# Optimization experiments

Measured on AMD Instinct MI355X. Metric: run time of the kernel, lower is better.

Reference implementation:

```python
import jax, jax.numpy as jnp
import numpy as np

B, NCH, NT = 64, 129, 200
D_MODEL, D_STATE, D_CONV, HEADDIM, NLAYERS = 256, 16, 4, 32, 4
D_INNER = 2 * D_MODEL            # expand=2 -> 512
NHEADS = D_INNER // HEADDIM      # 16
CONV_DIM = D_INNER + 2 * D_STATE # 544 (ngroups=1)
D_IN_PROJ = 2 * D_INNER + 2 * D_STATE + NHEADS  # 1072


def silu(x):
    return x * jax.nn.sigmoid(x)


def layernorm(x, w, b, eps=1e-5):
    m = x.mean(-1, keepdims=True)
    v = ((x - m) ** 2).mean(-1, keepdims=True)
    return (x - m) * jax.lax.rsqrt(v + eps) * w + b


def dwconv(x, w, b, pad):
    # x: (B, C, T), w: (C, K) depthwise, pad: (left, right)
    y = jax.lax.conv_general_dilated(x, w[:, None, :], (1,), [pad],
                                     feature_group_count=x.shape[1])
    return y + b[None, :, None]


def mamba2_block(u, Wi, cw, cb, dtb, Alog, Dh, nw, Wo):
    # u: (b, l, d_model)
    b, l, _ = u.shape
    zxbcdt = u @ Wi.T  # (b, l, 1072)
    z, xBC, dt = jnp.split(zxbcdt, [D_INNER, D_INNER + CONV_DIM], axis=-1)
    dt = jax.nn.softplus(dt + dtb)  # (b, l, nheads)
    # causal depthwise conv + silu on xBC
    xBC = silu(dwconv(xBC.transpose(0, 2, 1), cw, cb, (D_CONV - 1, 0)).transpose(0, 2, 1))
    xh, Bm, Cm = jnp.split(xBC, [D_INNER, D_INNER + D_STATE], axis=-1)
    xh = xh.reshape(b, l, NHEADS, HEADDIM)
    A = -jnp.exp(Alog)              # (h,)
    dA = jnp.exp(dt * A)            # (b, l, h)
    dtx = dt[..., None] * xh        # (b, l, h, p)

    def step(hst, inp):
        dA_t, dtx_t, B_t, C_t = inp
        hst = dA_t[:, :, None, None] * hst + dtx_t[..., None] * B_t[:, None, None, :]
        y_t = jnp.einsum('bhpn,bn->bhp', hst, C_t)
        return hst, y_t

    h0 = jnp.zeros((b, NHEADS, HEADDIM, D_STATE), u.dtype)
    _, ys = jax.lax.scan(step, h0, (dA.swapaxes(0, 1), dtx.swapaxes(0, 1),
                                    Bm.swapaxes(0, 1), Cm.swapaxes(0, 1)))
    y = ys.swapaxes(0, 1) + xh * Dh[None, None, :, None]  # (b, l, h, p)
    y = y.reshape(b, l, D_INNER)
    # gated RMSNorm (norm_before_gate=False): gate first, then rmsnorm
    y = y * silu(z)
    y = y * jax.lax.rsqrt((y * y).mean(-1, keepdims=True) + 1e-5) * nw
    return y @ Wo.T


def setup_inputs() -> dict:
    key = jax.random.key(0)
    ks = iter(jax.random.split(key, 32))
    nrm = lambda shape, s=0.02: jax.random.normal(next(ks), shape, jnp.float32) * s
    dt0 = jax.random.uniform(next(ks), (NLAYERS, NHEADS), minval=1e-3, maxval=0.1)
    return {
        'x': jax.random.normal(next(ks), (B, NCH, NT), jnp.float32),
        'emb': nrm((NCH, D_MODEL), 1.0),
        'sconv_w': nrm((NCH, 3), 0.3),
        'sconv_b': jnp.zeros((NCH,), jnp.float32),
        'mixer_w': nrm((D_MODEL, NCH), 0.05),
        'mixer_b': jnp.zeros((D_MODEL,), jnp.float32),
        'enc_ln_w': jnp.ones((D_MODEL,), jnp.float32),
        'enc_ln_b': jnp.zeros((D_MODEL,), jnp.float32),
        'in_proj_w': nrm((NLAYERS, D_IN_PROJ, D_MODEL)),
        'conv_w': nrm((NLAYERS, CONV_DIM, D_CONV), 0.3),
        'conv_b': jnp.zeros((NLAYERS, CONV_DIM), jnp.float32),
        'dt_bias': jnp.log(jnp.expm1(dt0)),
        'A_log': jnp.log(jax.random.uniform(next(ks), (NLAYERS, NHEADS), minval=1.0, maxval=16.0)),
        'D_skip': jnp.ones((NLAYERS, NHEADS), jnp.float32),
        'norm_w': jnp.ones((NLAYERS, D_INNER), jnp.float32),
        'out_proj_w': nrm((NLAYERS, D_MODEL, D_INNER)),
        'ln_w': jnp.ones((NLAYERS, D_MODEL), jnp.float32),
        'ln_b': jnp.zeros((NLAYERS, D_MODEL), jnp.float32),
        'head1_w': nrm((D_MODEL // 2, D_MODEL), 0.05),
        'head1_b': jnp.zeros((D_MODEL // 2,), jnp.float32),
        'head2_w': nrm((1, D_MODEL // 2), 0.05),
        'head2_b': jnp.zeros((1,), jnp.float32),
    }


def reference(x, emb, sconv_w, sconv_b, mixer_w, mixer_b, enc_ln_w, enc_ln_b,
              in_proj_w, conv_w, conv_b, dt_bias, A_log, D_skip, norm_w,
              out_proj_w, ln_w, ln_b, head1_w, head1_b, head2_w, head2_b):
    # SpatialChannelEncoder: depthwise conv over time + channel-mixing Linear
    xs = dwconv(x, sconv_w, sconv_b, (1, 1))                  # (b, c, t)
    h = jnp.einsum('bct,dc->btd', xs, mixer_w) + mixer_b      # (b, t, d)
    h = h + emb.mean(0)                                       # mean channel embedding
    h = layernorm(h, enc_ln_w, enc_ln_b)                      # dropout=identity (eval)
    # Stacked Mamba2 blocks with post-norm residual
    for i in range(NLAYERS):
        res = h
        y = mamba2_block(h, in_proj_w[i], conv_w[i], conv_b[i], dt_bias[i],
                         A_log[i], D_skip[i], norm_w[i], out_proj_w[i])
        h = layernorm(y + res, ln_w[i], ln_b[i])
    pooled = h.mean(1)                                        # AdaptiveAvgPool1d(1)
    hid = jax.nn.relu(pooled @ head1_w.T + head1_b)
    return hid @ head2_w.T + head2_b                          # (b, 1)
```

## Files before the change

kernel.cpp:

```cpp
#include <hip/hip_runtime.h>
#include <math.h>

#define B_   64
#define T_   200
#define DM   256
#define DI   512
#define NH   16
#define HD   32
#define DSZ  16
#define CD   544
#define DIP  1072
#define M_TOT (B_*T_)
#define NCH_ 129
#define KENC 192
#define NCHUNK 10
#define CLEN  20
#define NBC  48

typedef unsigned short u16;
typedef unsigned int u32;
typedef _Float16 f16;
typedef __attribute__((ext_vector_type(8))) _Float16 half8;
typedef __attribute__((ext_vector_type(4))) short short4v;
typedef __attribute__((ext_vector_type(4))) float f32x4;
typedef __attribute__((ext_vector_type(2))) float f32x2;

__device__ __forceinline__ float wave_sum(float v) {
    #pragma unroll
    for (int off = 32; off > 0; off >>= 1) v += __shfl_xor(v, off);
    return v;
}
__device__ __forceinline__ u16 f16bits(float a) {
    f16 h = (f16)a;
    return __builtin_bit_cast(u16, h);
}
__device__ __forceinline__ float f16tof(u16 v) {
    return (float)__builtin_bit_cast(f16, v);
}

__global__ void emb_mean_k(const float* __restrict__ emb, float* __restrict__ em) {
    int d = threadIdx.x;
    float s = 0.f;
    for (int c = 0; c < NCH_; ++c) s += emb[c * DM + d];
    em[d] = s * (1.f / NCH_);
}

__global__ void xsA2_k(const float* __restrict__ x, const float* __restrict__ w,
                       const float* __restrict__ b, u16* __restrict__ A2) {
    int idx = blockIdx.x * blockDim.x + threadIdx.x;
    if (idx >= M_TOT * KENC) return;
    int c = idx % KENC;
    int m = idx / KENC;
    float acc = 0.f;
    if (c < NCH_) {
        int t = m % T_;
        int bb = m / T_;
        const float* xr = x + (size_t)(bb * NCH_ + c) * T_;
        acc = b[c];
        if (t > 0)      acc += w[c*3+0] * xr[t-1];
        acc += w[c*3+1] * xr[t];
        if (t < T_-1)   acc += w[c*3+2] * xr[t+1];
    }
    A2[(size_t)m * KENC + c] = f16bits(acc);
}

__global__ void pack_b2s_k(const float* __restrict__ W, u16* __restrict__ B2,
                           int L, int N, int Npad, int Kreal, int K) {
    int idx = blockIdx.x * blockDim.x + threadIdx.x;
    if (idx >= L * Npad * K) return;
    int k = idx % K;
    int n = (idx / K) % Npad;
    int l = idx / (K * Npad);
    u16 hi = 0;
    if (n < N && k < Kreal)
        hi = f16bits(W[((size_t)l * N + n) * Kreal + k]);
    B2[((size_t)l * Npad + n) * K + k] = hi;
}

__global__ __launch_bounds__(256) void gemm_m64n128h(const u16* __restrict__ A2,
                                                     const u16* __restrict__ B2,
                                                     u16* __restrict__ C,
                                                     int K2, int ldc, int Nreal,
                                                     int nbx) {
    __shared__ u16 As[64 * 64];
    __shared__ u16 Bs[128 * 64];
    int nwg = gridDim.x;
    int lin = blockIdx.x;
    int q = nwg >> 3, r = nwg & 7;
    int xcd = lin & 7, idx = lin >> 3;
    int wg = ((xcd < r) ? xcd * (q + 1) : r * (q + 1) + (xcd - r) * q) + idx;
    int bx = wg % nbx, by = wg / nbx;

    int tid = threadIdx.x;
    int lane = tid & 63;
    int wave = tid >> 6;
    int wr = wave >> 1;
    int wc = wave & 1;
    int bm = by * 64;
    int bn = bx * 128;

    f32x4 acc[2][4] = {};
    const size_t ldA = (size_t)K2 * 2;

    for (int k0 = 0; k0 < K2; k0 += 64) {
        #pragma unroll
        for (int c = 0; c < 2; ++c) {
            int o = c * 4096 + tid * 16;
            int row = o >> 7;
            int slot = (o >> 4) & 7;
            int ss = slot ^ (row & 7);
            const char* src = (const char*)A2 + (size_t)(bm + row) * ldA
                              + (size_t)k0 * 2 + ss * 16;
            __builtin_amdgcn_global_load_lds(
                (const __attribute__((address_space(1))) u32*)src,
                (__attribute__((address_space(3))) u32*)((char*)As + o),
                16, 0, 0);
        }
        #pragma unroll
        for (int c = 0; c < 4; ++c) {
            int o = c * 4096 + tid * 16;
            int row = o >> 7;
            int slot = (o >> 4) & 7;
            int ss = slot ^ (row & 7);
            const char* src = (const char*)B2 + (size_t)(bn + row) * ldA
                              + (size_t)k0 * 2 + ss * 16;
            __builtin_amdgcn_global_load_lds(
                (const __attribute__((address_space(1))) u32*)src,
                (__attribute__((address_space(3))) u32*)((char*)Bs + o),
                16, 0, 0);
        }
        __syncthreads();
        #pragma unroll
        for (int kk = 0; kk < 2; ++kk) {
            int lslot = kk * 4 + (lane >> 4);
            half8 afr[2], bfr[4];
            #pragma unroll
            for (int n = 0; n < 4; ++n) {
                int row = wc * 64 + n * 16 + (lane & 15);
                int ps = lslot ^ (row & 7);
                bfr[n] = *(const half8*)((const char*)Bs + row * 128 + ps * 16);
            }
            #pragma unroll
            for (int m = 0; m < 2; ++m) {
                int row = wr * 32 + m * 16 + (lane & 15);
                int ps = lslot ^ (row & 7);
                afr[m] = *(const half8*)((const char*)As + row * 128 + ps * 16);
            }
            #pragma unroll
            for (int m = 0; m < 2; ++m)
                #pragma unroll
                for (int n = 0; n < 4; ++n)
                    acc[m][n] = __builtin_amdgcn_mfma_f32_16x16x32_f16(
                        bfr[n], afr[m], acc[m][n], 0, 0, 0);
        }
        __syncthreads();
    }

    int crow0 = bm + wr * 32;
    int ccol0 = bn + wc * 64;
    #pragma unroll
    for (int m = 0; m < 2; ++m) {
        int row = crow0 + m * 16 + (lane & 15);
        #pragma unroll
        for (int n = 0; n < 4; ++n) {
            int col = ccol0 + n * 16 + (lane >> 4) * 4;
            if (col < Nreal) {
                short4v hv;
                #pragma unroll
                for (int j = 0; j < 4; ++j) hv[j] = (short)f16bits(acc[m][n][j]);
                *(short4v*)(C + (size_t)row * ldc + col) = hv;
            }
        }
    }
}

__global__ __launch_bounds__(256) void gemm_m64n64(const u16* __restrict__ A2,
                                                   const u16* __restrict__ B2,
                                                   float* __restrict__ C,
                                                   int K2, int ldc, int Nreal,
                                                   int nbx) {
    __shared__ u16 As[64 * 64];
    __shared__ u16 Bs[64 * 64];
    int nwg = gridDim.x;
    int lin = blockIdx.x;
    int q = nwg >> 3, r = nwg & 7;
    int xcd = lin & 7, idx = lin >> 3;
    int wg = ((xcd < r) ? xcd * (q + 1) : r * (q + 1) + (xcd - r) * q) + idx;
    int bx = wg % nbx, by = wg / nbx;

    int tid = threadIdx.x;
    int lane = tid & 63;
    int wave = tid >> 6;
    int wr = wave >> 1;
    int wc = wave & 1;
    int bm = by * 64;
    int bn = bx * 64;

    f32x4 acc[2][2] = {};
    const size_t ldA = (size_t)K2 * 2;

    for (int k0 = 0; k0 < K2; k0 += 64) {
        #pragma unroll
        for (int c = 0; c < 2; ++c) {
            int o = c * 4096 + tid * 16;
            int row = o >> 7;
            int slot = (o >> 4) & 7;
            int ss = slot ^ (row & 7);
            const char* src = (const char*)A2 + (size_t)(bm + row) * ldA
                              + (size_t)k0 * 2 + ss * 16;
            __builtin_amdgcn_global_load_lds(
                (const __attribute__((address_space(1))) u32*)src,
                (__attribute__((address_space(3))) u32*)((char*)As + o),
                16, 0, 0);
        }
        #pragma unroll
        for (int c = 0; c < 2; ++c) {
            int o = c * 4096 + tid * 16;
            int row = o >> 7;
            int slot = (o >> 4) & 7;
            int ss = slot ^ (row & 7);
            const char* src = (const char*)B2 + (size_t)(bn + row) * ldA
                              + (size_t)k0 * 2 + ss * 16;
            __builtin_amdgcn_global_load_lds(
                (const __attribute__((address_space(1))) u32*)src,
                (__attribute__((address_space(3))) u32*)((char*)Bs + o),
                16, 0, 0);
        }
        __syncthreads();
        #pragma unroll
        for (int kk = 0; kk < 2; ++kk) {
            int lslot = kk * 4 + (lane >> 4);
            half8 afr[2], bfr[2];
            #pragma unroll
            for (int n = 0; n < 2; ++n) {
                int row = wc * 32 + n * 16 + (lane & 15);
                int ps = lslot ^ (row & 7);
                bfr[n] = *(const half8*)((const char*)Bs + row * 128 + ps * 16);
            }
            #pragma unroll
            for (int m = 0; m < 2; ++m) {
                int row = wr * 32 + m * 16 + (lane & 15);
                int ps = lslot ^ (row & 7);
                afr[m] = *(const half8*)((const char*)As + row * 128 + ps * 16);
            }
            #pragma unroll
            for (int m = 0; m < 2; ++m)
                #pragma unroll
                for (int n = 0; n < 2; ++n)
                    acc[m][n] = __builtin_amdgcn_mfma_f32_16x16x32_f16(
                        bfr[n], afr[m], acc[m][n], 0, 0, 0);
        }
        __syncthreads();
    }

    int crow0 = bm + wr * 32;
    int ccol0 = bn + wc * 32;
    #pragma unroll
    for (int m = 0; m < 2; ++m) {
        int row = crow0 + m * 16 + (lane & 15);
        #pragma unroll
        for (int n = 0; n < 2; ++n) {
            int col = ccol0 + n * 16 + (lane >> 4) * 4;
            if (col < Nreal)
                *(f32x4*)(C + (size_t)row * ldc + col) = acc[m][n];
        }
    }
}

__global__ __launch_bounds__(256) void gemm_m64n64h(const u16* __restrict__ A2,
                                                    const u16* __restrict__ B2,
                                                    u16* __restrict__ C,
                                                    int K2, int ldc, int Nreal,
                                                    int nbx) {
    __shared__ u16 As[64 * 64];
    __shared__ u16 Bs[64 * 64];
    int nwg = gridDim.x;
    int lin = blockIdx.x;
    int q = nwg >> 3, r = nwg & 7;
    int xcd = lin & 7, idx = lin >> 3;
    int wg = ((xcd < r) ? xcd * (q + 1) : r * (q + 1) + (xcd - r) * q) + idx;
    int bx = wg % nbx, by = wg / nbx;

    int tid = threadIdx.x;
    int lane = tid & 63;
    int wave = tid >> 6;
    int wr = wave >> 1;
    int wc = wave & 1;
    int bm = by * 64;
    int bn = bx * 64;

    f32x4 acc[2][2] = {};
    const size_t ldA = (size_t)K2 * 2;

    for (int k0 = 0; k0 < K2; k0 += 64) {
        #pragma unroll
        for (int c = 0; c < 2; ++c) {
            int o = c * 4096 + tid * 16;
            int row = o >> 7;
            int slot = (o >> 4) & 7;
            int ss = slot ^ (row & 7);
            const char* src = (const char*)A2 + (size_t)(bm + row) * ldA
                              + (size_t)k0 * 2 + ss * 16;
            __builtin_amdgcn_global_load_lds(
                (const __attribute__((address_space(1))) u32*)src,
                (__attribute__((address_space(3))) u32*)((char*)As + o),
                16, 0, 0);
        }
        #pragma unroll
        for (int c = 0; c < 2; ++c) {
            int o = c * 4096 + tid * 16;
            int row = o >> 7;
            int slot = (o >> 4) & 7;
            int ss = slot ^ (row & 7);
            const char* src = (const char*)B2 + (size_t)(bn + row) * ldA
                              + (size_t)k0 * 2 + ss * 16;
            __builtin_amdgcn_global_load_lds(
                (const __attribute__((address_space(1))) u32*)src,
                (__attribute__((address_space(3))) u32*)((char*)Bs + o),
                16, 0, 0);
        }
        __syncthreads();
        #pragma unroll
        for (int kk = 0; kk < 2; ++kk) {
            int lslot = kk * 4 + (lane >> 4);
            half8 afr[2], bfr[2];
            #pragma unroll
            for (int n = 0; n < 2; ++n) {
                int row = wc * 32 + n * 16 + (lane & 15);
                int ps = lslot ^ (row & 7);
                bfr[n] = *(const half8*)((const char*)Bs + row * 128 + ps * 16);
            }
            #pragma unroll
            for (int m = 0; m < 2; ++m) {
                int row = wr * 32 + m * 16 + (lane & 15);
                int ps = lslot ^ (row & 7);
                afr[m] = *(const half8*)((const char*)As + row * 128 + ps * 16);
            }
            #pragma unroll
            for (int m = 0; m < 2; ++m)
                #pragma unroll
                for (int n = 0; n < 2; ++n)
                    acc[m][n] = __builtin_amdgcn_mfma_f32_16x16x32_f16(
                        bfr[n], afr[m], acc[m][n], 0, 0, 0);
        }
        __syncthreads();
    }

    int crow0 = bm + wr * 32;
    int ccol0 = bn + wc * 32;
    #pragma unroll
    for (int m = 0; m < 2; ++m) {
        int row = crow0 + m * 16 + (lane & 15);
        #pragma unroll
        for (int n = 0; n < 2; ++n) {
            int col = ccol0 + n * 16 + (lane >> 4) * 4;
            if (col < Nreal) {
                short4v hv;
                #pragma unroll
                for (int j = 0; j < 4; ++j) hv[j] = (short)f16bits(acc[m][n][j]);
                *(short4v*)(C + (size_t)row * ldc + col) = hv;
            }
        }
    }
}

__global__ __launch_bounds__(256) void enc_ln_k(float* __restrict__ h,
        const float* __restrict__ mb, const float* __restrict__ em,
        const float* __restrict__ w, const float* __restrict__ bb,
        u16* __restrict__ A2) {
    int row = blockIdx.x * 4 + (threadIdx.x >> 6);
    int lane = threadIdx.x & 63;
    int e = lane * 4;
    float* hr = h + (size_t)row * DM;
    f32x4 v = *(const f32x4*)(hr + e);
    f32x4 vm = *(const f32x4*)(mb + e);
    f32x4 ve = *(const f32x4*)(em + e);
    float s = 0.f, sq = 0.f;
    #pragma unroll
    for (int j = 0; j < 4; ++j) {
        v[j] += vm[j] + ve[j];
        s += v[j];
        sq += v[j] * v[j];
    }
    s = wave_sum(s); sq = wave_sum(sq);
    float mean = s * (1.f / DM);
    float var = sq * (1.f / DM) - mean * mean;
    float r = rsqrtf(var + 1e-5f);
    f32x4 vw = *(const f32x4*)(w + e);
    f32x4 vb = *(const f32x4*)(bb + e);
    f32x4 o;
    short4v hi4;
    #pragma unroll
    for (int j = 0; j < 4; ++j) {
        float ov = (v[j] - mean) * r * vw[j] + vb[j];
        o[j] = ov;
        hi4[j] = (short)f16bits(ov);
    }
    *(f32x4*)(hr + e) = o;
    *(short4v*)(A2 + (size_t)row * 256 + e) = hi4;
}

__global__ void bc_dt_k(const u16* __restrict__ zx, const float* __restrict__ cw,
                        const float* __restrict__ cb, const float* __restrict__ dtb_in,
                        const float* __restrict__ A_log,
                        float* __restrict__ xbcs, float* __restrict__ dtdA) {
    int idx = blockIdx.x * blockDim.x + threadIdx.x;
    if (idx >= M_TOT * NBC) return;
    int c = idx % NBC;
    int m = idx / NBC;
    if (c < 32) {
        int cc = 512 + c;
        int t = m % T_;
        float acc = cb[cc];
        #pragma unroll
        for (int k = 0; k < 4; ++k) {
            int tt = t - 3 + k;
            if (tt >= 0)
                acc += cw[cc*4+k] * f16tof(zx[(size_t)(m - (3 - k)) * DIP + DI + cc]);
        }
        xbcs[(size_t)m * NBC + c] = acc / (1.f + expf(-acc));
    } else {
        int h = c - 32;
        float xv = f16tof(zx[(size_t)m * DIP + DI + CD + h]) + dtb_in[h];
        float dt = (xv > 20.f) ? xv : log1pf(expf(xv));
        float A = -expf(A_log[h]);
        f32x2 dd; dd[0] = dt; dd[1] = expf(dt * A);
        *(f32x2*)(dtdA + (size_t)(m * NH + h) * 2) = dd;
    }
}

__global__ __launch_bounds__(128) void scan1_k(const u16* __restrict__ zx,
        const float* __restrict__ xbcs, const float* __restrict__ dtdA,
        const float* __restrict__ cw, const float* __restrict__ cb,
        const float* __restrict__ D_skip,
        float* __restrict__ y, float* __restrict__ S, float* __restrict__ Pprod) {
    int c   = blockIdx.x % NCHUNK;
    int bhq = blockIdx.x / NCHUNK;
    int b   = bhq >> 2;
    int hq  = bhq & 3;
    int h   = hq * 4 + (threadIdx.x >> 5);
    int p   = threadIdx.x & 31;
    int ch  = h * HD + p;
    float Dh = D_skip[h];
    float w0 = cw[ch*4+0], w1 = cw[ch*4+1], w2 = cw[ch*4+2], w3 = cw[ch*4+3];
    float cbb = cb[ch];
    float s[16];
    #pragma unroll
    for (int n = 0; n < 16; ++n) s[n] = 0.f;
    float pr = 1.f;
    int t0 = c * CLEN;
    int base = b * T_ + t0;
    const u16* xsrc = zx + (size_t)base * DIP + DI + ch;
    float xm3 = (t0 >= 3) ? f16tof(xsrc[-3 * (ptrdiff_t)DIP]) : 0.f;
    float xm2 = (t0 >= 2) ? f16tof(xsrc[-2 * (ptrdiff_t)DIP]) : 0.f;
    float xm1 = (t0 >= 1) ? f16tof(xsrc[-1 * (ptrdiff_t)DIP]) : 0.f;
    float x0  = f16tof(xsrc[0]);
    f32x2 dd = *(const f32x2*)(dtdA + (size_t)(base * NH + h) * 2);
    float dt = dd[0], dA = dd[1];
    const float* bcr = xbcs + (size_t)base * NBC;
    f32x4 Bv[4], Cv[4];
    #pragma unroll
    for (int qq = 0; qq < 4; ++qq) {
        Bv[qq] = *(const f32x4*)(bcr + qq * 4);
        Cv[qq] = *(const f32x4*)(bcr + 16 + qq * 4);
    }
    for (int t = 0; t < CLEN; ++t) {
        int m = base + t;
        int tn = (t + 1 < CLEN) ? t + 1 : t;
        float x0n = f16tof(xsrc[(size_t)tn * DIP]);
        f32x2 ddn = *(const f32x2*)(dtdA + (size_t)((base + tn) * NH + h) * 2);
        const float* bcn = xbcs + (size_t)(base + tn) * NBC;
        f32x4 Bn_[4], Cn_[4];
        #pragma unroll
        for (int qq = 0; qq < 4; ++qq) {
            Bn_[qq] = *(const f32x4*)(bcn + qq * 4);
            Cn_[qq] = *(const f32x4*)(bcn + 16 + qq * 4);
        }
        float a = cbb + w0 * xm3 + w1 * xm2 + w2 * xm1 + w3 * x0;
        float xh = a / (1.f + expf(-a));
        pr *= dA;
        float dtx = dt * xh;
        float ya0 = 0.f, ya1 = 0.f, ya2 = 0.f, ya3 = 0.f;
        #pragma unroll
        for (int qq = 0; qq < 4; ++qq) {
            #pragma unroll
            for (int j = 0; j < 4; ++j) {
                int n = qq * 4 + j;
                s[n] = fmaf(dA, s[n], dtx * Bv[qq][j]);
                float prod = s[n] * Cv[qq][j];
                if (qq == 0) ya0 += prod;
                else if (qq == 1) ya1 += prod;
                else if (qq == 2) ya2 += prod;
                else ya3 += prod;
            }
        }
        y[(size_t)m * DI + ch] = fmaf(Dh, xh, (ya0 + ya1) + (ya2 + ya3));
        xm3 = xm2; xm2 = xm1; xm1 = x0; x0 = x0n;
        dt = ddn[0]; dA = ddn[1];
        #pragma unroll
        for (int qq = 0; qq < 4; ++qq) { Bv[qq] = Bn_[qq]; Cv[qq] = Cn_[qq]; }
    }
    size_t sidx = ((((size_t)b * NH + h) * NCHUNK + c) * 32 + p) * 16;
    #pragma unroll
    for (int qq = 0; qq < 4; ++qq) {
        f32x4 v; v[0]=s[qq*4]; v[1]=s[qq*4+1]; v[2]=s[qq*4+2]; v[3]=s[qq*4+3];
        *(f32x4*)(S + sidx + qq * 4) = v;
    }
    if (p == 0) Pprod[(b * NH + h) * NCHUNK + c] = pr;
}

__global__ __launch_bounds__(128) void scan3_k(const float* __restrict__ xbcs,
        const float* __restrict__ dtdA, const float* __restrict__ S,
        const float* __restrict__ Pprod, float* __restrict__ y) {
    int c   = (blockIdx.x % (NCHUNK - 1)) + 1;
    int bhq = blockIdx.x / (NCHUNK - 1);
    int b   = bhq >> 2;
    int hq  = bhq & 3;
    int h   = hq * 4 + (threadIdx.x >> 5);
    int p   = threadIdx.x & 31;
    size_t bh = (size_t)b * NH + h;
    float si[16];
    #pragma unroll
    for (int n = 0; n < 16; ++n) si[n] = 0.f;
    float wgt = 1.f;
    for (int j = c - 1; j >= 0; --j) {
        size_t eidx = ((bh * NCHUNK + j) * 32 + p) * 16;
        #pragma unroll
        for (int qq = 0; qq < 4; ++qq) {
            f32x4 e = *(const f32x4*)(S + eidx + qq * 4);
            #pragma unroll
            for (int jj = 0; jj < 4; ++jj)
                si[qq*4+jj] = fmaf(wgt, e[jj], si[qq*4+jj]);
        }
        wgt *= Pprod[bh * NCHUNK + j];
    }
    float cum = 1.f;
    int base = b * T_ + c * CLEN;
    for (int t = 0; t < CLEN; ++t) {
        int m = base + t;
        f32x2 dd = *(const f32x2*)(dtdA + (size_t)(m * NH + h) * 2);
        cum *= dd[1];
        const float* Cr = xbcs + (size_t)m * NBC + 16;
        float dot = 0.f;
        #pragma unroll
        for (int qq = 0; qq < 4; ++qq) {
            f32x4 Cv = *(const f32x4*)(Cr + qq * 4);
            #pragma unroll
            for (int jj = 0; jj < 4; ++jj) dot = fmaf(si[qq*4+jj], Cv[jj], dot);
        }
        y[(size_t)m * DI + h * HD + p] += cum * dot;
    }
}

__global__ __launch_bounds__(256) void gate_rms_k(const float* __restrict__ y,
        const u16* __restrict__ zx, const float* __restrict__ nw,
        u16* __restrict__ A2) {
    int row = blockIdx.x * 4 + (threadIdx.x >> 6);
    int lane = threadIdx.x & 63;
    int e0 = lane * 4, e1 = 256 + lane * 4;
    const float* yr = y + (size_t)row * DI;
    const u16* zr = zx + (size_t)row * DIP;
    f32x4 y0 = *(const f32x4*)(yr + e0);
    f32x4 y1 = *(const f32x4*)(yr + e1);
    short4v zh0 = *(const short4v*)(zr + e0);
    short4v zh1 = *(const short4v*)(zr + e1);
    f32x4 g0, g1;
    float sq = 0.f;
    #pragma unroll
    for (int j = 0; j < 4; ++j) {
        float z0 = f16tof((u16)zh0[j]);
        float z1 = f16tof((u16)zh1[j]);
        g0[j] = y0[j] * (z0 / (1.f + expf(-z0)));
        g1[j] = y1[j] * (z1 / (1.f + expf(-z1)));
        sq += g0[j] * g0[j] + g1[j] * g1[j];
    }
    sq = wave_sum(sq);
    float r = rsqrtf(sq * (1.f / DI) + 1e-5f);
    f32x4 w0 = *(const f32x4*)(nw + e0);
    f32x4 w1 = *(const f32x4*)(nw + e1);
    u16* ar = A2 + (size_t)row * 512;
    short4v hi4;
    #pragma unroll
    for (int j = 0; j < 4; ++j)
        hi4[j] = (short)f16bits(g0[j] * r * w0[j]);
    *(short4v*)(ar + e0) = hi4;
    #pragma unroll
    for (int j = 0; j < 4; ++j)
        hi4[j] = (short)f16bits(g1[j] * r * w1[j]);
    *(short4v*)(ar + e1) = hi4;
}

__global__ __launch_bounds__(256) void add_ln_k(float* __restrict__ h,
        const u16* __restrict__ c, const float* __restrict__ w,
        const float* __restrict__ bb, u16* __restrict__ A2) {
    int row = blockIdx.x * 4 + (threadIdx.x >> 6);
    int lane = threadIdx.x & 63;
    int e = lane * 4;
    float* hr = h + (size_t)row * DM;
    const u16* cr = c + (size_t)row * DM;
    f32x4 v = *(const f32x4*)(hr + e);
    short4v ch4 = *(const short4v*)(cr + e);
    float s = 0.f, sq = 0.f;
    #pragma unroll
    for (int j = 0; j < 4; ++j) {
        v[j] += f16tof((u16)ch4[j]);
        s += v[j];
        sq += v[j] * v[j];
    }
    s = wave_sum(s); sq = wave_sum(sq);
    float mean = s * (1.f / DM);
    float var = sq * (1.f / DM) - mean * mean;
    float r = rsqrtf(var + 1e-5f);
    f32x4 vw = *(const f32x4*)(w + e);
    f32x4 vb = *(const f32x4*)(bb + e);
    f32x4 o;
    short4v hi4;
    #pragma unroll
    for (int j = 0; j < 4; ++j) {
        float ov = (v[j] - mean) * r * vw[j] + vb[j];
        o[j] = ov;
        hi4[j] = (short)f16bits(ov);
    }
    *(f32x4*)(hr + e) = o;
    *(short4v*)(A2 + (size_t)row * 256 + e) = hi4;
}

__global__ __launch_bounds__(256) void pool_head_k(const float* __restrict__ h,
        const float* __restrict__ w1, const float* __restrict__ b1,
        const float* __restrict__ w2, const float* __restrict__ b2,
        float* __restrict__ out) {
    __shared__ float pl[DM];
    __shared__ float red[2];
    int b = blockIdx.x, tid = threadIdx.x;
    float s = 0.f;
    for (int t = 0; t < T_; ++t) s += h[(size_t)(b * T_ + t) * DM + tid];
    pl[tid] = s * (1.f / T_);
    __syncthreads();
    float v = 0.f;
    if (tid < 128) {
        float acc = b1[tid];
        #pragma unroll 4
        for (int d = 0; d < DM; ++d) acc = fmaf(pl[d], w1[tid * DM + d], acc);
        v = fmaxf(acc, 0.f) * w2[tid];
    }
    #pragma unroll
    for (int off = 32; off > 0; off >>= 1) v += __shfl_xor(v, off);
    if (tid == 0) red[0] = v;
    if (tid == 64) red[1] = v;
    __syncthreads();
    if (tid == 0) out[b] = red[0] + red[1] + b2[0];
}

extern "C" void kernel_launch(void* const* d_in, const int* in_sizes, int n_in,
                              void* d_out, int out_size, void* d_ws, size_t ws_size,
                              hipStream_t stream) {
    const float* x         = (const float*)d_in[0];
    const float* emb       = (const float*)d_in[1];
    const float* sconv_w   = (const float*)d_in[2];
    const float* sconv_b   = (const float*)d_in[3];
    const float* mixer_w   = (const float*)d_in[4];
    const float* mixer_b   = (const float*)d_in[5];
    const float* enc_ln_w  = (const float*)d_in[6];
    const float* enc_ln_b  = (const float*)d_in[7];
    const float* in_proj_w = (const float*)d_in[8];
    const float* conv_w    = (const float*)d_in[9];
    const float* conv_b    = (const float*)d_in[10];
    const float* dt_bias   = (const float*)d_in[11];
    const float* A_log     = (const float*)d_in[12];
    const float* D_skip    = (const float*)d_in[13];
    const float* norm_w    = (const float*)d_in[14];
    const float* out_proj_w= (const float*)d_in[15];
    const float* ln_w      = (const float*)d_in[16];
    const float* ln_b      = (const float*)d_in[17];
    const float* head1_w   = (const float*)d_in[18];
    const float* head1_b   = (const float*)d_in[19];
    const float* head2_w   = (const float*)d_in[20];
    const float* head2_b   = (const float*)d_in[21];
    float* out = (float*)d_out;

    float* ws  = (float*)d_ws;
    float* h    = ws;
    float* xbcs = h    + (size_t)M_TOT * DM;
    float* y    = xbcs + (size_t)M_TOT * NBC;
    float* dtdA = y    + (size_t)M_TOT * DI;
    float* em   = dtdA + (size_t)M_TOT * NH*2;
    float* S    = em + 256;
    float* Pprod = S + (size_t)B_*NH*NCHUNK*512;
    u16* zx   = (u16*)(Pprod + 10240);
    u16* cbuf = zx + (size_t)M_TOT * DIP;
    u16* A2   = cbuf + (size_t)M_TOT * DM;
    u16* B2e  = A2 + (size_t)M_TOT * 512;
    u16* B2i  = B2e + (size_t)256 * 192;
    u16* B2o  = B2i + (size_t)4 * 1152 * 256;

    emb_mean_k<<<1, DM, 0, stream>>>(emb, em);
    pack_b2s_k<<<(256 * KENC + 255) / 256, 256, 0, stream>>>(
        mixer_w, B2e, 1, DM, DM, NCH_, KENC);
    pack_b2s_k<<<(4 * 1152 * DM + 255) / 256, 256, 0, stream>>>(
        in_proj_w, B2i, 4, DIP, 1152, DM, DM);
    pack_b2s_k<<<(4 * 256 * DI + 255) / 256, 256, 0, stream>>>(
        out_proj_w, B2o, 4, DM, DM, DI, DI);

    xsA2_k<<<(M_TOT * KENC + 255) / 256, 256, 0, stream>>>(x, sconv_w, sconv_b, A2);
    gemm_m64n64<<<4 * 200, 256, 0, stream>>>(A2, B2e, h, KENC, DM, DM, 4);
    enc_ln_k<<<M_TOT / 4, 256, 0, stream>>>(h, mixer_b, em, enc_ln_w, enc_ln_b, A2);

    for (int l = 0; l < 4; ++l) {
        gemm_m64n128h<<<9 * 200, 256, 0, stream>>>(
            A2, B2i + (size_t)l * 1152 * 256, zx, 256, DIP, DIP, 9);

        bc_dt_k<<<(M_TOT * NBC + 255) / 256, 256, 0, stream>>>(
            zx, conv_w + l * CD * 4, conv_b + l * CD, dt_bias + l * NH,
            A_log + l * NH, xbcs, dtdA);

        scan1_k<<<B_ * 4 * NCHUNK, 128, 0, stream>>>(
            zx, xbcs, dtdA, conv_w + l * CD * 4, conv_b + l * CD,
            D_skip + l * NH, y, S, Pprod);
        scan3_k<<<B_ * 4 * (NCHUNK - 1), 128, 0, stream>>>(xbcs, dtdA, S, Pprod, y);

        gate_rms_k<<<M_TOT / 4, 256, 0, stream>>>(y, zx, norm_w + l * DI, A2);

        gemm_m64n64h<<<4 * 200, 256, 0, stream>>>(
            A2, B2o + (size_t)l * 256 * 512, cbuf, 512, DM, DM, 4);

        add_ln_k<<<M_TOT / 4, 256, 0, stream>>>(h, cbuf, ln_w + l * DM, ln_b + l * DM, A2);
    }

    pool_head_k<<<B_, 256, 0, stream>>>(h, head1_w, head1_b, head2_w, head2_b, out);
}
```

Measured before the change: 491.8 us.

## Fuse B/C conv and dt softplus into scan kernels via shared memory

Removes the separate bc_dt_k kernel and its xbcs/dtdA global buffers. Each scan1/scan3 block now computes the causal conv+SiLU for B/C and the dt/dA values for its chunk into shared memory, then reads them from LDS inside the time loop. This saves one launch per layer and a global write/read round trip. In exchange, B/C conv work is repeated across the 4 head-group blocks per batch and in scan3, and two block barriers are added.

Result: slower. 517.1 us (+5.1%).

```diff
diff --git a/kernel.cpp b/kernel.cpp
--- a/kernel.cpp
+++ b/kernel.cpp
@@ -15,7 +15,6 @@
 #define KENC 192
 #define NCHUNK 10
 #define CLEN  20
-#define NBC  48
 
 typedef unsigned short u16;
 typedef unsigned int u32;
@@ -23,7 +22,6 @@
 typedef __attribute__((ext_vector_type(8))) _Float16 half8;
 typedef __attribute__((ext_vector_type(4))) short short4v;
 typedef __attribute__((ext_vector_type(4))) float f32x4;
-typedef __attribute__((ext_vector_type(2))) float f32x2;
 
 __device__ __forceinline__ float wave_sum(float v) {
     #pragma unroll
@@ -400,47 +398,49 @@
     *(short4v*)(A2 + (size_t)row * 256 + e) = hi4;
 }
 
-__global__ void bc_dt_k(const u16* __restrict__ zx, const float* __restrict__ cw,
-                        const float* __restrict__ cb, const float* __restrict__ dtb_in,
-                        const float* __restrict__ A_log,
-                        float* __restrict__ xbcs, float* __restrict__ dtdA) {
-    int idx = blockIdx.x * blockDim.x + threadIdx.x;
-    if (idx >= M_TOT * NBC) return;
-    int c = idx % NBC;
-    int m = idx / NBC;
-    if (c < 32) {
-        int cc = 512 + c;
-        int t = m % T_;
-        float acc = cb[cc];
-        #pragma unroll
-        for (int k = 0; k < 4; ++k) {
-            int tt = t - 3 + k;
-            if (tt >= 0)
-                acc += cw[cc*4+k] * f16tof(zx[(size_t)(m - (3 - k)) * DIP + DI + cc]);
-        }
-        xbcs[(size_t)m * NBC + c] = acc / (1.f + expf(-acc));
-    } else {
-        int h = c - 32;
-        float xv = f16tof(zx[(size_t)m * DIP + DI + CD + h]) + dtb_in[h];
-        float dt = (xv > 20.f) ? xv : log1pf(expf(xv));
-        float A = -expf(A_log[h]);
-        f32x2 dd; dd[0] = dt; dd[1] = expf(dt * A);
-        *(f32x2*)(dtdA + (size_t)(m * NH + h) * 2) = dd;
-    }
-}
-
 __global__ __launch_bounds__(128) void scan1_k(const u16* __restrict__ zx,
-        const float* __restrict__ xbcs, const float* __restrict__ dtdA,
         const float* __restrict__ cw, const float* __restrict__ cb,
+        const float* __restrict__ dtb_in, const float* __restrict__ A_log,
         const float* __restrict__ D_skip,
         float* __restrict__ y, float* __restrict__ S, float* __restrict__ Pprod) {
+    __shared__ float zbc[CLEN + 3][32];
+    __shared__ float BCs[CLEN][32];
+    __shared__ float dtA[CLEN][4][2];
     int c   = blockIdx.x % NCHUNK;
     int bhq = blockIdx.x / NCHUNK;
     int b   = bhq >> 2;
     int hq  = bhq & 3;
-    int h   = hq * 4 + (threadIdx.x >> 5);
-    int p   = threadIdx.x & 31;
+    int tid = threadIdx.x;
+    int hl  = tid >> 5;
+    int h   = hq * 4 + hl;
+    int p   = tid & 31;
     int ch  = h * HD + p;
+    int t0  = c * CLEN;
+    int base = b * T_ + t0;
+
+    for (int i = tid; i < (CLEN + 3) * 32; i += 128) {
+        int tt = i >> 5, cc = i & 31;
+        int tg = t0 + tt - 3;
+        zbc[tt][cc] = (tg >= 0)
+            ? f16tof(zx[(size_t)(b * T_ + tg) * DIP + DI + 512 + cc]) : 0.f;
+    }
+    for (int i = tid; i < CLEN * 4; i += 128) {
+        int t = i >> 2, hh = hq * 4 + (i & 3);
+        float xv = f16tof(zx[(size_t)(base + t) * DIP + DI + CD + hh]) + dtb_in[hh];
+        float dtv = (xv > 20.f) ? xv : log1pf(expf(xv));
+        dtA[t][i & 3][0] = dtv;
+        dtA[t][i & 3][1] = expf(dtv * (-expf(A_log[hh])));
+    }
+    __syncthreads();
+    for (int i = tid; i < CLEN * 32; i += 128) {
+        int t = i >> 5, cc = i & 31;
+        int c2 = 512 + cc;
+        float acc = cb[c2] + cw[c2*4+0] * zbc[t][cc] + cw[c2*4+1] * zbc[t+1][cc]
+                  + cw[c2*4+2] * zbc[t+2][cc] + cw[c2*4+3] * zbc[t+3][cc];
+        BCs[t][cc] = acc / (1.f + expf(-acc));
+    }
+    __syncthreads();
+
     float Dh = D_skip[h];
     float w0 = cw[ch*4+0], w1 = cw[ch*4+1], w2 = cw[ch*4+2], w3 = cw[ch*4+3];
     float cbb = cb[ch];
@@ -448,34 +448,17 @@
     #pragma unroll
     for (int n = 0; n < 16; ++n) s[n] = 0.f;
     float pr = 1.f;
-    int t0 = c * CLEN;
-    int base = b * T_ + t0;
     const u16* xsrc = zx + (size_t)base * DIP + DI + ch;
     float xm3 = (t0 >= 3) ? f16tof(xsrc[-3 * (ptrdiff_t)DIP]) : 0.f;
     float xm2 = (t0 >= 2) ? f16tof(xsrc[-2 * (ptrdiff_t)DIP]) : 0.f;
     float xm1 = (t0 >= 1) ? f16tof(xsrc[-1 * (ptrdiff_t)DIP]) : 0.f;
     float x0  = f16tof(xsrc[0]);
-    f32x2 dd = *(const f32x2*)(dtdA + (size_t)(base * NH + h) * 2);
-    float dt = dd[0], dA = dd[1];
-    const float* bcr = xbcs + (size_t)base * NBC;
-    f32x4 Bv[4], Cv[4];
-    #pragma unroll
-    for (int qq = 0; qq < 4; ++qq) {
-        Bv[qq] = *(const f32x4*)(bcr + qq * 4);
-        Cv[qq] = *(const f32x4*)(bcr + 16 + qq * 4);
-    }
     for (int t = 0; t < CLEN; ++t) {
         int m = base + t;
         int tn = (t + 1 < CLEN) ? t + 1 : t;
         float x0n = f16tof(xsrc[(size_t)tn * DIP]);
-        f32x2 ddn = *(const f32x2*)(dtdA + (size_t)((base + tn) * NH + h) * 2);
-        const float* bcn = xbcs + (size_t)(base + tn) * NBC;
-        f32x4 Bn_[4], Cn_[4];
-        #pragma unroll
-        for (int qq = 0; qq < 4; ++qq) {
-            Bn_[qq] = *(const f32x4*)(bcn + qq * 4);
-            Cn_[qq] = *(const f32x4*)(bcn + 16 + qq * 4);
-        }
+        float dt = dtA[t][hl][0];
+        float dA = dtA[t][hl][1];
         float a = cbb + w0 * xm3 + w1 * xm2 + w2 * xm1 + w3 * x0;
         float xh = a / (1.f + expf(-a));
         pr *= dA;
@@ -483,11 +466,13 @@
         float ya0 = 0.f, ya1 = 0.f, ya2 = 0.f, ya3 = 0.f;
         #pragma unroll
         for (int qq = 0; qq < 4; ++qq) {
+            f32x4 Bv = *(const f32x4*)&BCs[t][qq * 4];
+            f32x4 Cv = *(const f32x4*)&BCs[t][16 + qq * 4];
             #pragma unroll
             for (int j = 0; j < 4; ++j) {
                 int n = qq * 4 + j;
-                s[n] = fmaf(dA, s[n], dtx * Bv[qq][j]);
-                float prod = s[n] * Cv[qq][j];
+                s[n] = fmaf(dA, s[n], dtx * Bv[j]);
+                float prod = s[n] * Cv[j];
                 if (qq == 0) ya0 += prod;
                 else if (qq == 1) ya1 += prod;
                 else if (qq == 2) ya2 += prod;
@@ -496,9 +481,6 @@
         }
         y[(size_t)m * DI + ch] = fmaf(Dh, xh, (ya0 + ya1) + (ya2 + ya3));
         xm3 = xm2; xm2 = xm1; xm1 = x0; x0 = x0n;
-        dt = ddn[0]; dA = ddn[1];
-        #pragma unroll
-        for (int qq = 0; qq < 4; ++qq) { Bv[qq] = Bn_[qq]; Cv[qq] = Cn_[qq]; }
     }
     size_t sidx = ((((size_t)b * NH + h) * NCHUNK + c) * 32 + p) * 16;
     #pragma unroll
@@ -509,16 +491,48 @@
     if (p == 0) Pprod[(b * NH + h) * NCHUNK + c] = pr;
 }
 
-__global__ __launch_bounds__(128) void scan3_k(const float* __restrict__ xbcs,
-        const float* __restrict__ dtdA, const float* __restrict__ S,
-        const float* __restrict__ Pprod, float* __restrict__ y) {
+__global__ __launch_bounds__(128) void scan3_k(const u16* __restrict__ zx,
+        const float* __restrict__ cw, const float* __restrict__ cb,
+        const float* __restrict__ dtb_in, const float* __restrict__ A_log,
+        const float* __restrict__ S, const float* __restrict__ Pprod,
+        float* __restrict__ y) {
+    __shared__ float zc[CLEN + 3][16];
+    __shared__ float Cs[CLEN][16];
+    __shared__ float dAs[CLEN][4];
     int c   = (blockIdx.x % (NCHUNK - 1)) + 1;
     int bhq = blockIdx.x / (NCHUNK - 1);
     int b   = bhq >> 2;
     int hq  = bhq & 3;
-    int h   = hq * 4 + (threadIdx.x >> 5);
-    int p   = threadIdx.x & 31;
+    int tid = threadIdx.x;
+    int hl  = tid >> 5;
+    int h   = hq * 4 + hl;
+    int p   = tid & 31;
+    int t0  = c * CLEN;
+    int base = b * T_ + t0;
     size_t bh = (size_t)b * NH + h;
+
+    for (int i = tid; i < (CLEN + 3) * 16; i += 128) {
+        int tt = i >> 4, cc = i & 15;
+        int tg = t0 + tt - 3;
+        zc[tt][cc] = (tg >= 0)
+            ? f16tof(zx[(size_t)(b * T_ + tg) * DIP + DI + 528 + cc]) : 0.f;
+    }
+    for (int i = tid; i < CLEN * 4; i += 128) {
+        int t = i >> 2, hh = hq * 4 + (i & 3);
+        float xv = f16tof(zx[(size_t)(base + t) * DIP + DI + CD + hh]) + dtb_in[hh];
+        float dtv = (xv > 20.f) ? xv : log1pf(expf(xv));
+        dAs[t][i & 3] = expf(dtv * (-expf(A_log[hh])));
+    }
+    __syncthreads();
+    for (int i = tid; i < CLEN * 16; i += 128) {
+        int t = i >> 4, cc = i & 15;
+        int c2 = 528 + cc;
+        float acc = cb[c2] + cw[c2*4+0] * zc[t][cc] + cw[c2*4+1] * zc[t+1][cc]
+                  + cw[c2*4+2] * zc[t+2][cc] + cw[c2*4+3] * zc[t+3][cc];
+        Cs[t][cc] = acc / (1.f + expf(-acc));
+    }
+    __syncthreads();
+
     float si[16];
     #pragma unroll
     for (int n = 0; n < 16; ++n) si[n] = 0.f;
@@ -535,16 +549,13 @@
         wgt *= Pprod[bh * NCHUNK + j];
     }
     float cum = 1.f;
-    int base = b * T_ + c * CLEN;
     for (int t = 0; t < CLEN; ++t) {
         int m = base + t;
-        f32x2 dd = *(const f32x2*)(dtdA + (size_t)(m * NH + h) * 2);
-        cum *= dd[1];
-        const float* Cr = xbcs + (size_t)m * NBC + 16;
+        cum *= dAs[t][hl];
         float dot = 0.f;
         #pragma unroll
         for (int qq = 0; qq < 4; ++qq) {
-            f32x4 Cv = *(const f32x4*)(Cr + qq * 4);
+            f32x4 Cv = *(const f32x4*)&Cs[t][qq * 4];
             #pragma unroll
             for (int jj = 0; jj < 4; ++jj) dot = fmaf(si[qq*4+jj], Cv[jj], dot);
         }
@@ -680,10 +691,8 @@
 
     float* ws  = (float*)d_ws;
     float* h    = ws;
-    float* xbcs = h    + (size_t)M_TOT * DM;
-    float* y    = xbcs + (size_t)M_TOT * NBC;
-    float* dtdA = y    + (size_t)M_TOT * DI;
-    float* em   = dtdA + (size_t)M_TOT * NH*2;
+    float* y    = h  + (size_t)M_TOT * DM;
+    float* em   = y  + (size_t)M_TOT * DI;
     float* S    = em + 256;
     float* Pprod = S + (size_t)B_*NH*NCHUNK*512;
     u16* zx   = (u16*)(Pprod + 10240);
@@ -709,14 +718,12 @@
         gemm_m64n128h<<<9 * 200, 256, 0, stream>>>(
             A2, B2i + (size_t)l * 1152 * 256, zx, 256, DIP, DIP, 9);
 
-        bc_dt_k<<<(M_TOT * NBC + 255) / 256, 256, 0, stream>>>(
+        scan1_k<<<B_ * 4 * NCHUNK, 128, 0, stream>>>(
             zx, conv_w + l * CD * 4, conv_b + l * CD, dt_bias + l * NH,
-            A_log + l * NH, xbcs, dtdA);
-
-        scan1_k<<<B_ * 4 * NCHUNK, 128, 0, stream>>>(
-            zx, xbcs, dtdA, conv_w + l * CD * 4, conv_b + l * CD,
-            D_skip + l * NH, y, S, Pprod);
-        scan3_k<<<B_ * 4 * (NCHUNK - 1), 128, 0, stream>>>(xbcs, dtdA, S, Pprod, y);
+            A_log + l * NH, D_skip + l * NH, y, S, Pprod);
+        scan3_k<<<B_ * 4 * (NCHUNK - 1), 128, 0, stream>>>(
+            zx, conv_w + l * CD * 4, conv_b + l * CD, dt_bias + l * NH,
+            A_log + l * NH, S, Pprod, y);
 
         gate_rms_k<<<M_TOT / 4, 256, 0, stream>>>(y, zx, norm_w + l * DI, A2);
 
```
